# Performance work log

Hardware: AMD Instinct MI355X
Metric: run time of the kernel (lower is better)

The kernel has to match this reference:

```python
import jax, jax.numpy as jnp
import numpy as np
from jax import lax

H = 128; NOISE = 128; L = 16; A = 10; HYB = 3; F_NODE = 17; E_FEAT = 4
TEMP = 1.0
MAX_VALENCES = jnp.array([4., 3., 2., 1., 4., 2., 6., 1., 4., 4.], dtype=jnp.float32)


def setup_inputs():
    key = jax.random.key(0)
    ks = jax.random.split(key, 16)
    B, N = 4096, 32
    def w(k, *s):
        return jax.random.normal(k, s, dtype=jnp.float32) * 0.05
    return {
        'noise': jax.random.normal(ks[0], (B, NOISE), dtype=jnp.float32),
        'w1': w(ks[1], NOISE, H), 'b1': jnp.zeros((H,), jnp.float32),
        'gat_w': w(ks[2], L, H, H), 'gat_b': jnp.zeros((L, H), jnp.float32),
        'att_src': w(ks[3], L, H), 'att_dst': w(ks[4], L, H),
        'w_atom': w(ks[5], H, A), 'b_atom': jnp.zeros((A,), jnp.float32),
        'w_hyb': w(ks[6], H, HYB), 'b_hyb': jnp.zeros((HYB,), jnp.float32),
        'w_deg': w(ks[7], H, 1), 'b_deg': jnp.zeros((1,), jnp.float32),
        'w_chg': w(ks[8], H, 1), 'b_chg': jnp.zeros((1,), jnp.float32),
        'w_arom': w(ks[9], H, 1), 'b_arom': jnp.zeros((1,), jnp.float32),
        'w_eex': w(ks[10], 2 * F_NODE, 1), 'b_eex': jnp.zeros((1,), jnp.float32),
        'w_ety': w(ks[11], 2 * F_NODE, E_FEAT), 'b_ety': jnp.zeros((E_FEAT,), jnp.float32),
        'batch_size': B, 'num_nodes': N,
    }


def _gumbel(k, shape):
    u = jax.random.uniform(k, shape, minval=1e-6, maxval=1.0 - 1e-6)
    return -jnp.log(-jnp.log(u))


def reference(noise, w1, b1, gat_w, gat_b, att_src, att_dst, w_atom, b_atom,
              w_hyb, b_hyb, w_deg, b_deg, w_chg, b_chg, w_arom, b_arom,
              w_eex, b_eex, w_ety, b_ety, batch_size, num_nodes):
    B, N = batch_size, num_nodes
    h0 = jax.nn.relu(noise @ w1 + b1)                      # [B,H]
    x = jnp.broadcast_to(h0[:, None, :], (B, N, h0.shape[-1]))
    idx = jnp.arange(N)
    # chain adjacency (both directions) + self loops (PyG GATConv default)
    adj = (jnp.abs(idx[:, None] - idx[None, :]) == 1) | (idx[:, None] == idx[None, :])
    neg = jnp.float32(-1e9)

    def layer(xc, p):
        W, b, a_s, a_d = p
        h = xc @ W + b                                     # [B,N,H]
        e_src = h @ a_s                                    # [B,N]
        e_dst = h @ a_d
        s = jax.nn.leaky_relu(e_dst[:, :, None] + e_src[:, None, :], 0.2)  # [B,N,N]
        s = jnp.where(adj, s, neg)
        alpha = jax.nn.softmax(s, axis=-1)
        out = jnp.einsum('bij,bjh->bih', alpha, h)
        return jax.nn.relu(out + xc), None                 # residual GAT layer

    x, _ = lax.scan(layer, x, (gat_w, gat_b, att_src, att_dst))

    sk = jax.random.split(jax.random.key(42), 4)
    # atom type head + categorical sampling (Gumbel-max on logits/T)
    atom_logits = x @ w_atom + b_atom                      # [B,N,A]
    atom_lp = jax.nn.log_softmax(atom_logits, axis=-1)
    atom_idx = jnp.argmax(atom_logits / TEMP + _gumbel(sk[0], atom_logits.shape), axis=-1)
    atom_lp_mol = jnp.take_along_axis(atom_lp, atom_idx[..., None], axis=-1)[..., 0].mean(axis=1)
    # hybridization head
    hyb_logits = x @ w_hyb + b_hyb                         # [B,N,3]
    hyb_lp = jax.nn.log_softmax(hyb_logits, axis=-1)
    hyb_idx = jnp.argmax(hyb_logits / TEMP + _gumbel(sk[1], hyb_logits.shape), axis=-1)
    hyb_lp_mol = jnp.take_along_axis(hyb_lp, hyb_idx[..., None], axis=-1)[..., 0].mean(axis=1)
    # remaining node heads
    deg = jax.nn.sigmoid(x @ w_deg + b_deg)
    chg = jnp.tanh(lax.stop_gradient(x @ w_chg + b_chg))   # .clone().detach() in torch
    arom_p = jax.nn.sigmoid(x @ w_arom + b_arom)
    arom = (jax.random.uniform(sk[2], arom_p.shape) < arom_p).astype(jnp.float32)
    val = (MAX_VALENCES[atom_idx] / 5.0)[..., None]
    node_features = jnp.concatenate([
        jax.nn.one_hot(atom_idx, A, dtype=jnp.float32), deg, chg,
        jax.nn.one_hot(hyb_idx, HYB, dtype=jnp.float32), arom, val], axis=-1)  # [B,N,17]
    # edge heads on chain edges (both directions)
    u = jnp.arange(N - 1); v = u + 1
    eu = jnp.concatenate([u, v]); ev = jnp.concatenate([v, u])
    ef = jnp.concatenate([node_features[:, eu], node_features[:, ev]], axis=-1)  # [B,2(N-1),34]
    exist_p = jax.nn.sigmoid(ef @ w_eex + b_eex)[..., 0]
    edge_mask = exist_p > 0.5
    type_logits = ef @ w_ety + b_ety
    type_idx = jnp.argmax(type_logits / TEMP + _gumbel(sk[3], type_logits.shape), axis=-1)
    edge_attr = jax.nn.one_hot(type_idx, E_FEAT, dtype=jnp.float32)
    return node_features, atom_lp_mol, hyb_lp_mol, edge_attr, edge_mask
```

## Files before the change

### kernel.cpp

```cpp
#include <hip/hip_runtime.h>
#include <stdint.h>
#include <math.h>


typedef double d4 __attribute__((ext_vector_type(4)));

struct U2 { uint32_t a, b; };

__device__ __forceinline__ U2 threefry(uint32_t k0, uint32_t k1, uint32_t x0, uint32_t x1) {
  const uint32_t ks2 = k0 ^ k1 ^ 0x1BD11BDAu;
#define TFR(r) { x0 += x1; x1 = (x1 << (r)) | (x1 >> (32 - (r))); x1 ^= x0; }
  x0 += k0;  x1 += k1;
  TFR(13) TFR(15) TFR(26) TFR(6)
  x0 += k1;  x1 += ks2 + 1u;
  TFR(17) TFR(29) TFR(16) TFR(24)
  x0 += ks2; x1 += k0 + 2u;
  TFR(13) TFR(15) TFR(26) TFR(6)
  x0 += k0;  x1 += k1 + 3u;
  TFR(17) TFR(29) TFR(16) TFR(24)
  x0 += k1;  x1 += ks2 + 4u;
  TFR(13) TFR(15) TFR(26) TFR(6)
  x0 += ks2; x1 += k0 + 5u;
#undef TFR
  U2 r; r.a = x0; r.b = x1; return r;
}

__device__ __forceinline__ uint32_t pbits(uint32_t k0, uint32_t k1, uint32_t ctr) {
  U2 r = threefry(k0, k1, 0u, ctr);
  return r.a ^ r.b;
}

__device__ __forceinline__ float bits_to_unit(uint32_t bits) {
  return __uint_as_float((bits >> 9) | 0x3f800000u) - 1.0f;
}

__device__ __forceinline__ float jgumbel(uint32_t k0, uint32_t k1, uint32_t ctr) {
  const float minv = 1e-6f;
  const float maxv = (float)(1.0 - 1e-6);
  const float span = maxv - minv;
  float f = bits_to_unit(pbits(k0, k1, ctr));
  float u = fmaxf(minv, __fadd_rn(__fmul_rn(f, span), minv));
  return -logf(-logf(u));
}

extern "C" __global__ void __launch_bounds__(512)
gen_kernel(const float* __restrict__ noise,
           const float* __restrict__ w1,
           const float* __restrict__ b1,
           const float* __restrict__ gat_w,
           const float* __restrict__ gat_b,
           const float* __restrict__ w_atom,
           const float* __restrict__ b_atom,
           const float* __restrict__ w_hyb,
           const float* __restrict__ b_hyb,
           const float* __restrict__ w_deg,
           const float* __restrict__ b_deg,
           const float* __restrict__ w_chg,
           const float* __restrict__ b_chg,
           const float* __restrict__ w_arom,
           const float* __restrict__ b_arom,
           const float* __restrict__ w_eex,
           const float* __restrict__ b_eex,
           const float* __restrict__ w_ety,
           const float* __restrict__ b_ety,
           float* __restrict__ out)
{
  __shared__ __align__(16) double sX[2][128][18];
  __shared__ double sScr[16][16];
  __shared__ float  sNF[16][32][17];
  __shared__ double sLP[16][64];

  const int t       = threadIdx.x;
  const int wv      = t >> 6;
  const int ln      = t & 63;
  const int g       = ln >> 4;
  const int i       = ln & 15;
  const int molBase = blockIdx.x * 16;
  const int colb    = wv << 4;

  int rowOf[4], colOf[4];
  {
    d4 z4 = {0.0, 0.0, 0.0, 0.0};
    const double selK0 = (g == 0) ? 1.0 : 0.0;
    const double idxv  = (double)i;
    d4 prow = __builtin_amdgcn_mfma_f64_16x16x4f64(idxv,  selK0, z4, 0, 0, 0);
    d4 pcol = __builtin_amdgcn_mfma_f64_16x16x4f64(selK0, idxv,  z4, 0, 0, 0);
    #pragma unroll
    for (int j = 0; j < 4; ++j) {
      rowOf[j] = (int)prow[j];
      colOf[j] = (int)pcol[j];
    }
  }

  #pragma unroll
  for (int it = 0; it < 4; ++it) {
    const int idx = t + (it << 9);
    const int c = idx & 127, m = idx >> 7;
    sX[0][c][m] = (double)noise[(((size_t)(molBase + m)) << 7) + c];
  }
  __syncthreads();

  int p = 0;
  #pragma unroll 1
  for (int l = 0; l < 17; ++l) {
    const float* __restrict__ W  = (l == 0) ? w1 : (gat_w + (((size_t)(l - 1)) << 14));
    const float* __restrict__ bp = (l == 0) ? b1 : (gat_b + ((l - 1) << 7));
    const int q = p ^ 1;

    d4 acc = {0.0, 0.0, 0.0, 0.0};

    #pragma unroll
    for (int ks = 0; ks < 32; ++ks) {
      const int kk = (ks << 2) + g;
      const double a  = sX[p][kk][i];
      const double wb = (double)W[(kk << 7) + colb + i];
      acc = __builtin_amdgcn_mfma_f64_16x16x4f64(a, wb, acc, 0, 0, 0);
    }

    #pragma unroll
    for (int j = 0; j < 4; ++j) {
      const int cc = colb + colOf[j];
      double tv = acc[j] + (double)bp[cc];
      if (l > 0) tv += sX[p][cc][rowOf[j]];
      sX[q][cc][rowOf[j]] = fmax(tv, 0.0);
    }
    __syncthreads();
    p = q;
  }

  if (t < 256) {
    const int mh = t >> 4;
    const int h  = t & 15;
    const float* wp; int stride; double bias;
    if (h < 10)       { wp = w_atom + h;        stride = 10; bias = (double)b_atom[h]; }
    else if (h < 13)  { wp = w_hyb + (h - 10);  stride = 3;  bias = (double)b_hyb[h - 10]; }
    else if (h == 13) { wp = w_deg;             stride = 1;  bias = (double)b_deg[0]; }
    else if (h == 14) { wp = w_chg;             stride = 1;  bias = (double)b_chg[0]; }
    else              { wp = w_arom;            stride = 1;  bias = (double)b_arom[0]; }
    double acc = 0.0;
    for (int c = 0; c < 128; ++c)
      acc = fma(sX[p][c][mh], (double)wp[c * stride], acc);
    sScr[mh][h] = acc + bias;
  }
  __syncthreads();

  const U2 k0p = threefry(0u, 42u, 0u, 0u);
  const U2 k1p = threefry(0u, 42u, 0u, 1u);
  const U2 k2p = threefry(0u, 42u, 0u, 2u);
  const U2 k3p = threefry(0u, 42u, 0u, 3u);

  {
    const int mloc = t >> 5;
    const int n    = t & 31;
    const int mol  = molBase + mloc;
    const double* scr = sScr[mloc];

    double m = scr[0];
    #pragma unroll
    for (int a = 1; a < 10; ++a) m = fmax(m, scr[a]);
    double lsum = 0.0;
    #pragma unroll
    for (int a = 0; a < 10; ++a) lsum += exp(scr[a] - m);
    const double lse = log(lsum);
    const uint32_t abase = ((uint32_t)mol * 32u + (uint32_t)n) * 10u;
    int asel = 0; double abest = 0.0;
    #pragma unroll
    for (int a = 0; a < 10; ++a) {
      const double gg = (double)jgumbel(k0p.a, k0p.b, abase + (uint32_t)a);
      const double sc = scr[a] + gg;
      if (a == 0 || sc > abest) { abest = sc; asel = a; }
    }
    sLP[mloc][n] = (scr[asel] - m) - lse;

    double m2 = fmax(fmax(scr[10], scr[11]), scr[12]);
    double ls2 = exp(scr[10] - m2) + exp(scr[11] - m2) + exp(scr[12] - m2);
    const double lse2 = log(ls2);
    const uint32_t hbase = ((uint32_t)mol * 32u + (uint32_t)n) * 3u;
    int hsel = 0; double hbest = 0.0;
    #pragma unroll
    for (int j = 0; j < 3; ++j) {
      const double gg = (double)jgumbel(k1p.a, k1p.b, hbase + (uint32_t)j);
      const double sc = scr[10 + j] + gg;
      if (j == 0 || sc > hbest) { hbest = sc; hsel = j; }
    }
    sLP[mloc][32 + n] = (scr[10 + hsel] - m2) - lse2;

    const double deg = 1.0 / (1.0 + exp(-scr[13]));
    const double chg = tanh(scr[14]);
    const double pr  = 1.0 / (1.0 + exp(-scr[15]));
    const uint32_t ridx = (uint32_t)mol * 32u + (uint32_t)n;
    const double uu = (double)bits_to_unit(pbits(k2p.a, k2p.b, ridx));
    const double arom = (uu < pr) ? 1.0 : 0.0;
    const double valt[10] = {4.0/5.0, 3.0/5.0, 2.0/5.0, 1.0/5.0, 4.0/5.0,
                             2.0/5.0, 6.0/5.0, 1.0/5.0, 4.0/5.0, 4.0/5.0};
    double nf[17];
    #pragma unroll
    for (int q2 = 0; q2 < 10; ++q2) nf[q2] = (q2 == asel) ? 1.0 : 0.0;
    nf[10] = deg; nf[11] = chg;
    #pragma unroll
    for (int j = 0; j < 3; ++j) nf[12 + j] = (j == hsel) ? 1.0 : 0.0;
    nf[15] = arom; nf[16] = valt[asel];

    const size_t o = ((size_t)mol * 32 + n) * 17;
    #pragma unroll
    for (int q2 = 0; q2 < 17; ++q2) {
      sNF[mloc][n][q2] = (float)nf[q2];
      out[o + q2] = (float)nf[q2];
    }
  }
  __syncthreads();

  #pragma unroll 1
  for (int r = 0; r < 2; ++r) {
    const int mloc = (r << 3) + wv;
    const int mol  = molBase + mloc;
    if (ln == 62) {
      double sa = 0.0;
      for (int n = 0; n < 32; ++n) sa += sLP[mloc][n];
      out[2228224 + (size_t)mol] = (float)(sa / 32.0);
    } else if (ln == 63) {
      double sh = 0.0;
      for (int n = 0; n < 32; ++n) sh += sLP[mloc][32 + n];
      out[2232320 + (size_t)mol] = (float)(sh / 32.0);
    } else {
      const int e = ln;
      const int nu_ = (e < 31) ? e : (e - 30);
      const int nv_ = (e < 31) ? (e + 1) : (e - 31);
      double lex = 0.0;
      double lt[4] = {0.0, 0.0, 0.0, 0.0};
      for (int q2 = 0; q2 < 17; ++q2) {
        const double f = (double)sNF[mloc][nu_][q2];
        lex = fma(f, (double)w_eex[q2], lex);
        #pragma unroll
        for (int c = 0; c < 4; ++c) lt[c] = fma(f, (double)w_ety[q2 * 4 + c], lt[c]);
      }
      for (int q2 = 0; q2 < 17; ++q2) {
        const double f = (double)sNF[mloc][nv_][q2];
        lex = fma(f, (double)w_eex[17 + q2], lex);
        #pragma unroll
        for (int c = 0; c < 4; ++c) lt[c] = fma(f, (double)w_ety[(17 + q2) * 4 + c], lt[c]);
      }
      lex += (double)b_eex[0];
      #pragma unroll
      for (int c = 0; c < 4; ++c) lt[c] += (double)b_ety[c];

      const double pex = 1.0 / (1.0 + exp(-lex));
      out[3252224 + (size_t)mol * 62 + e] = (pex > 0.5) ? 1.f : 0.f;

      const uint32_t tbase = ((uint32_t)mol * 62u + (uint32_t)e) * 4u;
      int tsel = 0; double tbest = 0.0;
      #pragma unroll
      for (int c = 0; c < 4; ++c) {
        const double gg = (double)jgumbel(k3p.a, k3p.b, tbase + (uint32_t)c);
        const double sc = lt[c] + gg;
        if (c == 0 || sc > tbest) { tbest = sc; tsel = c; }
      }
      const size_t o = 2236416 + ((size_t)mol * 62 + e) * 4;
      #pragma unroll
      for (int c = 0; c < 4; ++c) out[o + c] = (c == tsel) ? 1.f : 0.f;
    }
  }
}

extern "C" void kernel_launch(void* const* d_in, const int* in_sizes, int n_in,
                              void* d_out, int out_size, void* d_ws, size_t ws_size,
                              hipStream_t stream) {
  (void)in_sizes; (void)n_in; (void)out_size; (void)d_ws; (void)ws_size;
  hipLaunchKernelGGL(gen_kernel, dim3(256), dim3(512), 0, stream,
                     (const float*)d_in[0],  (const float*)d_in[1],
                     (const float*)d_in[2],  (const float*)d_in[3],
                     (const float*)d_in[4],
                     (const float*)d_in[7],  (const float*)d_in[8],
                     (const float*)d_in[9],  (const float*)d_in[10],
                     (const float*)d_in[11], (const float*)d_in[12],
                     (const float*)d_in[13], (const float*)d_in[14],
                     (const float*)d_in[15], (const float*)d_in[16],
                     (const float*)d_in[17], (const float*)d_in[18],
                     (const float*)d_in[19], (const float*)d_in[20],
                     (float*)d_out);
}
```

Baseline: 178.7 us.

## Prefetch next layer weights into registers and split MFMA accumulator chains

Double-buffers each layer's weight column slice in registers, loading the next layer's weights before issuing the current layer's MFMAs so global-load latency overlaps compute. The single serial accumulator chain is also split into four independent accumulators, which breaks the MFMA dependency chain. This raises register pressure (64 extra floats per thread) and may lower occupancy. It also changes the fp64 summation order slightly.

```diff
diff --git a/kernel.cpp b/kernel.cpp
--- a/kernel.cpp
+++ b/kernel.cpp
@@ -92,6 +92,12 @@
     }
   }
 
+  float wr0[32], wr1[32];
+
+  #pragma unroll
+  for (int ks = 0; ks < 32; ++ks)
+    wr0[ks] = w1[(((ks << 2) + g) << 7) + colb + i];
+
   #pragma unroll
   for (int it = 0; it < 4; ++it) {
     const int idx = t + (it << 9);
@@ -101,32 +107,50 @@
   __syncthreads();
 
   int p = 0;
+
+#define LAYERSTEP(WUSE, WPRE, nextWptr, bptr, ISFIRST)                          \
+  {                                                                             \
+    const int q = p ^ 1;                                                        \
+    const float* __restrict__ nW = (nextWptr);                                  \
+    _Pragma("unroll")                                                           \
+    for (int ks = 0; ks < 32; ++ks)                                             \
+      WPRE[ks] = nW[(((ks << 2) + g) << 7) + colb + i];                         \
+    d4 ac0 = {0.0,0.0,0.0,0.0}, ac1 = {0.0,0.0,0.0,0.0};                        \
+    d4 ac2 = {0.0,0.0,0.0,0.0}, ac3 = {0.0,0.0,0.0,0.0};                        \
+    _Pragma("unroll")                                                           \
+    for (int ks = 0; ks < 32; ks += 4) {                                        \
+      ac0 = __builtin_amdgcn_mfma_f64_16x16x4f64(sX[p][((ks + 0) << 2) + g][i], \
+            (double)WUSE[ks + 0], ac0, 0, 0, 0);                                \
+      ac1 = __builtin_amdgcn_mfma_f64_16x16x4f64(sX[p][((ks + 1) << 2) + g][i], \
+            (double)WUSE[ks + 1], ac1, 0, 0, 0);                                \
+      ac2 = __builtin_amdgcn_mfma_f64_16x16x4f64(sX[p][((ks + 2) << 2) + g][i], \
+            (double)WUSE[ks + 2], ac2, 0, 0, 0);                                \
+      ac3 = __builtin_amdgcn_mfma_f64_16x16x4f64(sX[p][((ks + 3) << 2) + g][i], \
+            (double)WUSE[ks + 3], ac3, 0, 0, 0);                                \
+    }                                                                           \
+    _Pragma("unroll")                                                           \
+    for (int j = 0; j < 4; ++j) {                                               \
+      const int cc = colb + colOf[j];                                           \
+      double tv = ((ac0[j] + ac1[j]) + (ac2[j] + ac3[j])) + (double)(bptr)[cc]; \
+      if (!(ISFIRST)) tv += sX[p][cc][rowOf[j]];                                \
+      sX[q][cc][rowOf[j]] = fmax(tv, 0.0);                                      \
+    }                                                                           \
+    __syncthreads();                                                            \
+    p = q;                                                                      \
+  }
+
+  LAYERSTEP(wr0, wr1, gat_w, b1, 1)
+
   #pragma unroll 1
-  for (int l = 0; l < 17; ++l) {
-    const float* __restrict__ W  = (l == 0) ? w1 : (gat_w + (((size_t)(l - 1)) << 14));
-    const float* __restrict__ bp = (l == 0) ? b1 : (gat_b + ((l - 1) << 7));
-    const int q = p ^ 1;
-
-    d4 acc = {0.0, 0.0, 0.0, 0.0};
-
-    #pragma unroll
-    for (int ks = 0; ks < 32; ++ks) {
-      const int kk = (ks << 2) + g;
-      const double a  = sX[p][kk][i];
-      const double wb = (double)W[(kk << 7) + colb + i];
-      acc = __builtin_amdgcn_mfma_f64_16x16x4f64(a, wb, acc, 0, 0, 0);
-    }
-
-    #pragma unroll
-    for (int j = 0; j < 4; ++j) {
-      const int cc = colb + colOf[j];
-      double tv = acc[j] + (double)bp[cc];
-      if (l > 0) tv += sX[p][cc][rowOf[j]];
-      sX[q][cc][rowOf[j]] = fmax(tv, 0.0);
-    }
-    __syncthreads();
-    p = q;
-  }
+  for (int li = 0; li < 8; ++li) {
+    const int lA = 2 * li;
+    const int lB = 2 * li + 1;
+    const int pfA = lB;
+    const int pfB = (lB + 1 < 16) ? (lB + 1) : 15;
+    LAYERSTEP(wr1, wr0, gat_w + ((size_t)pfA << 14), gat_b + (lA << 7), 0)
+    LAYERSTEP(wr0, wr1, gat_w + ((size_t)pfB << 14), gat_b + (lB << 7), 0)
+  }
+#undef LAYERSTEP
 
   if (t < 256) {
     const int mh = t >> 4;
```

Result: no change. 177.9 us (-0.5%).
